# Kernel tuning notes

Measured on AMD Instinct MI355X. Metric: run time of the kernel, lower is better.

## Reference

```python
import jax, jax.numpy as jnp
import numpy as np

H = 1024
F = 4096  # base_ffn_dim = hidden * 4
WIDTHS = [256, 512]  # adapters; idx 2 -> width==hidden -> identity
EPS = 1e-5


def _xavier(key, fan_in, fan_out, gain):
    a = gain * np.sqrt(6.0 / (fan_in + fan_out))
    return jax.random.uniform(key, (fan_in, fan_out), jnp.float32, -a, a)


def _layernorm(x, g, b):
    mu = jnp.mean(x, axis=-1, keepdims=True)
    var = jnp.var(x, axis=-1, keepdims=True)
    return (x - mu) * jax.lax.rsqrt(var + EPS) * g + b


def setup_inputs() -> dict:
    key = jax.random.key(0)
    ks = jax.random.split(key, 12)
    g = 1.0 / np.sqrt(2.0)
    B, S = 4, 2048
    return {
        "x": jax.random.normal(ks[0], (B, S, H), jnp.float32),
        "width_multiplier": jax.random.uniform(ks[1], (B, S, 1), jnp.float32),
        "width_idx": jax.random.randint(ks[2], (B, S), 0, 3, jnp.int32),
        "ln_in_g": jnp.ones((H,), jnp.float32),
        "ln_in_b": jnp.zeros((H,), jnp.float32),
        "W1": _xavier(ks[3], H, F, g),
        "b1": jnp.zeros((F,), jnp.float32),
        "ln_h_g": jnp.ones((F,), jnp.float32),
        "ln_h_b": jnp.zeros((F,), jnp.float32),
        "W2": _xavier(ks[4], F, H, g),
        "b2": jnp.zeros((H,), jnp.float32),
        "a256_w1": _xavier(ks[5], H, 256, g),
        "a256_b1": jnp.zeros((256,), jnp.float32),
        "a256_w2": _xavier(ks[6], 256, H, g),
        "a256_b2": jnp.zeros((H,), jnp.float32),
        "a512_w1": _xavier(ks[7], H, 512, g),
        "a512_b1": jnp.zeros((512,), jnp.float32),
        "a512_w2": _xavier(ks[8], 512, H, g),
        "a512_b2": jnp.zeros((H,), jnp.float32),
    }


def reference(x, width_multiplier, width_idx,
              ln_in_g, ln_in_b, W1, b1, ln_h_g, ln_h_b, W2, b2,
              a256_w1, a256_b1, a256_w2, a256_b2,
              a512_w1, a512_b1, a512_w2, a512_b2):
    gelu = lambda t: jax.nn.gelu(t, approximate=False)  # torch nn.GELU exact
    x_norm = _layernorm(x, ln_in_g, ln_in_b)
    # base FFN path
    h = gelu(jnp.einsum("bsh,hf->bsf", x_norm, W1) + b1)
    h = _layernorm(h, ln_h_g, ln_h_b)
    base = jnp.einsum("bsf,fh->bsh", h, W2) + b2
    # width adapters (routed per token by width_idx)
    ad0 = jnp.einsum("bsw,wh->bsh", gelu(jnp.einsum("bsh,hw->bsw", x_norm, a256_w1) + a256_b1), a256_w2) + a256_b2
    ad1 = jnp.einsum("bsw,wh->bsh", gelu(jnp.einsum("bsh,hw->bsw", x_norm, a512_w1) + a512_b1), a512_w2) + a512_b2
    idx = width_idx[..., None]
    adaptive = jnp.where(idx == 0, ad0, jnp.where(idx == 1, ad1, x_norm))
    return base * width_multiplier + adaptive * (1.0 - width_multiplier)
```

## Files before the change

### kernel.cpp

```cpp
#include <hip/hip_runtime.h>
#include <cstdint>
#include <cstddef>

typedef unsigned short u16x8 __attribute__((ext_vector_type(8)));
typedef __bf16 bf16x8 __attribute__((ext_vector_type(8)));
typedef float f32x4 __attribute__((ext_vector_type(4)));

__device__ __forceinline__ float b2f(unsigned short u) {
    union { unsigned int i; float f; } v;
    v.i = ((unsigned int)u) << 16;
    return v.f;
}

__device__ __forceinline__ unsigned short f2b(float f) {
    union { float f; unsigned int i; } v;
    v.f = f;
    unsigned int x = v.i;
    unsigned int lsb = (x >> 16) & 1u;
    x += 0x7FFFu + lsb;
    return (unsigned short)(x >> 16);
}

__device__ __forceinline__ float gelu_exact(float x) {
    return 0.5f * x * (1.0f + erff(x * 0.70710678118654752f));
}

__global__ void transpose_f32_bf16(const float* __restrict__ in,
                                   unsigned short* __restrict__ out, int R, int C) {
    __shared__ float tile[32][33];
    int x = blockIdx.x * 32 + threadIdx.x;
    int y0 = blockIdx.y * 32;
    for (int k = 0; k < 32; k += 8)
        tile[threadIdx.y + k][threadIdx.x] = in[(size_t)(y0 + threadIdx.y + k) * C + x];
    __syncthreads();
    int ox = y0 + threadIdx.x;
    int oy = blockIdx.x * 32;
    for (int k = 0; k < 32; k += 8)
        out[(size_t)(oy + threadIdx.y + k) * R + ox] = f2b(tile[threadIdx.x][threadIdx.y + k]);
}

__device__ __forceinline__ float ldf(const float* p, int i) { return p[i]; }
__device__ __forceinline__ float ldf(const unsigned short* p, int i) { return b2f(p[i]); }

template <int NPT, typename TIN>
__global__ __launch_bounds__(256) void ln_rows(const TIN* __restrict__ in,
                                               unsigned short* __restrict__ out,
                                               const float* __restrict__ g,
                                               const float* __restrict__ b) {
    const int ncol = NPT * 256;
    const int row = blockIdx.x;
    const int t = threadIdx.x;
    const TIN* xr = in + (size_t)row * ncol;

    float v[NPT];
    float s = 0.f, s2 = 0.f;
#pragma unroll
    for (int i = 0; i < NPT; ++i) {
        float f = ldf(xr, t + (i << 8));
        v[i] = f;
        s += f;
        s2 += f * f;
    }
#pragma unroll
    for (int o = 32; o > 0; o >>= 1) {
        s  += __shfl_down(s, o, 64);
        s2 += __shfl_down(s2, o, 64);
    }
    __shared__ float red[8];
    int lane = t & 63, w = t >> 6;
    if (lane == 0) { red[w] = s; red[4 + w] = s2; }
    __syncthreads();
    if (t == 0) {
        red[0] = red[0] + red[1] + red[2] + red[3];
        red[4] = red[4] + red[5] + red[6] + red[7];
    }
    __syncthreads();
    float inv_n = 1.0f / (float)ncol;
    float mu = red[0] * inv_n;
    float var = red[4] * inv_n - mu * mu;
    float rs = rsqrtf(var + 1e-5f);

    unsigned short* orow = out + (size_t)row * ncol;
#pragma unroll
    for (int i = 0; i < NPT; ++i) {
        int c = t + (i << 8);
        orow[c] = f2b((v[i] - mu) * rs * g[c] + b[c]);
    }
}

#define LDSS 40

template <int EPI>
__global__ __launch_bounds__(256) void gemm_bt(
    const unsigned short* __restrict__ A, const unsigned short* __restrict__ BT,
    const float* __restrict__ bias, unsigned short* __restrict__ Cb,
    float* __restrict__ Cf, int M, int N, int K,
    const int* __restrict__ idx, int match,
    const float* __restrict__ wm,
    const unsigned short* __restrict__ adaptive,
    const unsigned short* __restrict__ xn) {
    __shared__ __align__(16) unsigned short As[128 * LDSS];
    __shared__ __align__(16) unsigned short Bs[128 * LDSS];

    const int t = threadIdx.x;
    const int m0 = blockIdx.y * 128;
    const int n0 = blockIdx.x * 128;

    const int r0 = t >> 2;
    const int kk = (t & 3) << 3;

    const int lane = t & 63;
    const int wid = t >> 6;
    const int wr = (wid >> 1) << 6;
    const int wc = (wid & 1) << 6;
    const int ml = lane & 15;
    const int q = lane >> 4;

    f32x4 acc[4][4];
#pragma unroll
    for (int i = 0; i < 4; ++i)
#pragma unroll
        for (int j = 0; j < 4; ++j)
#pragma unroll
            for (int r = 0; r < 4; ++r) acc[i][j][r] = 0.0f;

    for (int k0 = 0; k0 < K; k0 += 32) {
#pragma unroll
        for (int hh = 0; hh < 2; ++hh) {
            int row = r0 + (hh << 6);
            *(u16x8*)(&As[row * LDSS + kk]) =
                *(const u16x8*)(A + (size_t)(m0 + row) * K + k0 + kk);
            *(u16x8*)(&Bs[row * LDSS + kk]) =
                *(const u16x8*)(BT + (size_t)(n0 + row) * K + k0 + kk);
        }
        __syncthreads();

        bf16x8 af[4], bf[4];
#pragma unroll
        for (int i = 0; i < 4; ++i)
            af[i] = *(const bf16x8*)(&As[(wr + i * 16 + ml) * LDSS + (q << 3)]);
#pragma unroll
        for (int j = 0; j < 4; ++j)
            bf[j] = *(const bf16x8*)(&Bs[(wc + j * 16 + ml) * LDSS + (q << 3)]);
#pragma unroll
        for (int i = 0; i < 4; ++i)
#pragma unroll
            for (int j = 0; j < 4; ++j)
                acc[i][j] = __builtin_amdgcn_mfma_f32_16x16x32_bf16(af[i], bf[j], acc[i][j], 0, 0, 0);
        __syncthreads();
    }

#pragma unroll
    for (int i = 0; i < 4; ++i) {
#pragma unroll
        for (int j = 0; j < 4; ++j) {
            int col = n0 + wc + j * 16 + ml;
            float bv = bias[col];
#pragma unroll
            for (int r = 0; r < 4; ++r) {
                int row = m0 + wr + i * 16 + q * 4 + r;
                float val = acc[i][j][r] + bv;
                size_t off = (size_t)row * N + col;
                if (EPI == 0) {
                    Cb[off] = f2b(gelu_exact(val));
                } else if (EPI == 1) {
                    if (idx[row] == match) Cb[off] = f2b(val);
                } else {
                    float w = wm[row];
                    int id = idx[row];
                    float a = b2f((id <= 1) ? adaptive[off] : xn[off]);
                    Cf[off] = val * w + a * (1.0f - w);
                }
            }
        }
    }
}

extern "C" void kernel_launch(void* const* d_in, const int* in_sizes, int n_in,
                              void* d_out, int out_size, void* d_ws, size_t ws_size,
                              hipStream_t stream) {
    const float* x       = (const float*)d_in[0];
    const float* wm      = (const float*)d_in[1];
    const int*   widx    = (const int*)d_in[2];
    const float* ln_in_g = (const float*)d_in[3];
    const float* ln_in_b = (const float*)d_in[4];
    const float* W1      = (const float*)d_in[5];
    const float* b1      = (const float*)d_in[6];
    const float* ln_h_g  = (const float*)d_in[7];
    const float* ln_h_b  = (const float*)d_in[8];
    const float* W2      = (const float*)d_in[9];
    const float* b2      = (const float*)d_in[10];
    const float* a256_w1 = (const float*)d_in[11];
    const float* a256_b1 = (const float*)d_in[12];
    const float* a256_w2 = (const float*)d_in[13];
    const float* a256_b2 = (const float*)d_in[14];
    const float* a512_w1 = (const float*)d_in[15];
    const float* a512_b1 = (const float*)d_in[16];
    const float* a512_w2 = (const float*)d_in[17];
    const float* a512_b2 = (const float*)d_in[18];
    float* out = (float*)d_out;

    const int T = 8192, H = 1024, F = 4096;

    unsigned short* ws0   = (unsigned short*)d_ws;
    unsigned short* xn    = ws0;
    unsigned short* h     = xn    + (size_t)T * H;
    unsigned short* t0    = h     + (size_t)T * F;
    unsigned short* t1    = t0    + (size_t)T * 256;
    unsigned short* adp   = t1    + (size_t)T * 512;
    unsigned short* W1T   = adp   + (size_t)T * H;
    unsigned short* W2T   = W1T   + (size_t)H * F;
    unsigned short* aw1T0 = W2T   + (size_t)F * H;
    unsigned short* aw2T0 = aw1T0 + (size_t)256 * H;
    unsigned short* aw1T1 = aw2T0 + (size_t)H * 256;
    unsigned short* aw2T1 = aw1T1 + (size_t)512 * H;

    dim3 tb(32, 8);
    transpose_f32_bf16<<<dim3(F / 32,   H / 32), tb, 0, stream>>>(W1,      W1T,   H,   F);
    transpose_f32_bf16<<<dim3(H / 32,   F / 32), tb, 0, stream>>>(W2,      W2T,   F,   H);
    transpose_f32_bf16<<<dim3(256 / 32, H / 32), tb, 0, stream>>>(a256_w1, aw1T0, H,   256);
    transpose_f32_bf16<<<dim3(H / 32, 256 / 32), tb, 0, stream>>>(a256_w2, aw2T0, 256, H);
    transpose_f32_bf16<<<dim3(512 / 32, H / 32), tb, 0, stream>>>(a512_w1, aw1T1, H,   512);
    transpose_f32_bf16<<<dim3(H / 32, 512 / 32), tb, 0, stream>>>(a512_w2, aw2T1, 512, H);

    ln_rows<4, float><<<T, 256, 0, stream>>>(x, xn, ln_in_g, ln_in_b);

    gemm_bt<0><<<dim3(F / 128, T / 128), 256, 0, stream>>>(
        xn, W1T, b1, h, nullptr, T, F, H, nullptr, 0, nullptr, nullptr, nullptr);

    gemm_bt<0><<<dim3(256 / 128, T / 128), 256, 0, stream>>>(
        xn, aw1T0, a256_b1, t0, nullptr, T, 256, H, nullptr, 0, nullptr, nullptr, nullptr);
    gemm_bt<1><<<dim3(H / 128, T / 128), 256, 0, stream>>>(
        t0, aw2T0, a256_b2, adp, nullptr, T, H, 256, widx, 0, nullptr, nullptr, nullptr);

    gemm_bt<0><<<dim3(512 / 128, T / 128), 256, 0, stream>>>(
        xn, aw1T1, a512_b1, t1, nullptr, T, 512, H, nullptr, 0, nullptr, nullptr, nullptr);
    gemm_bt<1><<<dim3(H / 128, T / 128), 256, 0, stream>>>(
        t1, aw2T1, a512_b2, adp, nullptr, T, H, 512, widx, 1, nullptr, nullptr, nullptr);

    ln_rows<16, unsigned short><<<T, 256, 0, stream>>>(h, h, ln_h_g, ln_h_b);

    gemm_bt<2><<<dim3(H / 128, T / 128), 256, 0, stream>>>(
        h, W2T, b2, nullptr, out, T, H, F, widx, 0, wm, adp, xn);
}
```

Before: 507.3 us.

## Load GEMM tiles directly into LDS and fuse adapter up-projections

Global-to-shared tile loads in the GEMM now use the global_load_lds builtin, bypassing registers, and the padded LDS stride is replaced by an unpadded 32-element stride. Leading dimensions are passed as parameters so the two adapter up-projection GEMMs can be merged into a single N=768 GEMM, with the weights and biases concatenated. This aims to cut load instruction and register overhead and one kernel launch. The unpadded layout risks LDS bank conflicts on fragment reads.

```diff
diff --git a/kernel.cpp b/kernel.cpp
--- a/kernel.cpp
+++ b/kernel.cpp
@@ -23,6 +23,12 @@
 
 __device__ __forceinline__ float gelu_exact(float x) {
     return 0.5f * x * (1.0f + erff(x * 0.70710678118654752f));
+}
+
+__device__ __forceinline__ void ld_lds16(const unsigned short* g, unsigned short* l) {
+    __builtin_amdgcn_global_load_lds(
+        (const __attribute__((address_space(1))) void*)g,
+        (__attribute__((address_space(3))) void*)l, 16, 0, 0);
 }
 
 __global__ void transpose_f32_bf16(const float* __restrict__ in,
@@ -39,6 +45,13 @@
         out[(size_t)(oy + threadIdx.y + k) * R + ox] = f2b(tile[threadIdx.x][threadIdx.y + k]);
 }
 
+__global__ void concat_bias(const float* __restrict__ b0, const float* __restrict__ b1,
+                            float* __restrict__ out) {
+    int t = threadIdx.x + blockIdx.x * blockDim.x;
+    if (t < 256) out[t] = b0[t];
+    else if (t < 768) out[t] = b1[t - 256];
+}
+
 __device__ __forceinline__ float ldf(const float* p, int i) { return p[i]; }
 __device__ __forceinline__ float ldf(const unsigned short* p, int i) { return b2f(p[i]); }
 
@@ -88,29 +101,29 @@
     }
 }
 
-#define LDSS 40
-
 template <int EPI>
 __global__ __launch_bounds__(256) void gemm_bt(
-    const unsigned short* __restrict__ A, const unsigned short* __restrict__ BT,
+    const unsigned short* __restrict__ A, int lda,
+    const unsigned short* __restrict__ BT, int ldb,
     const float* __restrict__ bias, unsigned short* __restrict__ Cb,
     float* __restrict__ Cf, int M, int N, int K,
     const int* __restrict__ idx, int match,
     const float* __restrict__ wm,
     const unsigned short* __restrict__ adaptive,
     const unsigned short* __restrict__ xn) {
-    __shared__ __align__(16) unsigned short As[128 * LDSS];
-    __shared__ __align__(16) unsigned short Bs[128 * LDSS];
+    __shared__ __align__(16) unsigned short As[128 * 32];
+    __shared__ __align__(16) unsigned short Bs[128 * 32];
 
     const int t = threadIdx.x;
     const int m0 = blockIdx.y * 128;
     const int n0 = blockIdx.x * 128;
 
-    const int r0 = t >> 2;
-    const int kk = (t & 3) << 3;
-
     const int lane = t & 63;
     const int wid = t >> 6;
+
+    const int srow = lane >> 2;
+    const int scol = (lane & 3) << 3;
+
     const int wr = (wid >> 1) << 6;
     const int wc = (wid & 1) << 6;
     const int ml = lane & 15;
@@ -127,21 +140,20 @@
     for (int k0 = 0; k0 < K; k0 += 32) {
 #pragma unroll
         for (int hh = 0; hh < 2; ++hh) {
-            int row = r0 + (hh << 6);
-            *(u16x8*)(&As[row * LDSS + kk]) =
-                *(const u16x8*)(A + (size_t)(m0 + row) * K + k0 + kk);
-            *(u16x8*)(&Bs[row * LDSS + kk]) =
-                *(const u16x8*)(BT + (size_t)(n0 + row) * K + k0 + kk);
+            int rbase = wid * 32 + hh * 16;
+            int row = rbase + srow;
+            ld_lds16(A  + (size_t)(m0 + row) * lda + k0 + scol, &As[rbase * 32]);
+            ld_lds16(BT + (size_t)(n0 + row) * ldb + k0 + scol, &Bs[rbase * 32]);
         }
         __syncthreads();
 
         bf16x8 af[4], bf[4];
 #pragma unroll
         for (int i = 0; i < 4; ++i)
-            af[i] = *(const bf16x8*)(&As[(wr + i * 16 + ml) * LDSS + (q << 3)]);
+            af[i] = *(const bf16x8*)(&As[(wr + i * 16 + ml) * 32 + (q << 3)]);
 #pragma unroll
         for (int j = 0; j < 4; ++j)
-            bf[j] = *(const bf16x8*)(&Bs[(wc + j * 16 + ml) * LDSS + (q << 3)]);
+            bf[j] = *(const bf16x8*)(&Bs[(wc + j * 16 + ml) * 32 + (q << 3)]);
 #pragma unroll
         for (int i = 0; i < 4; ++i)
 #pragma unroll
@@ -205,41 +217,39 @@
     unsigned short* ws0   = (unsigned short*)d_ws;
     unsigned short* xn    = ws0;
     unsigned short* h     = xn    + (size_t)T * H;
-    unsigned short* t0    = h     + (size_t)T * F;
-    unsigned short* t1    = t0    + (size_t)T * 256;
-    unsigned short* adp   = t1    + (size_t)T * 512;
+    unsigned short* tt    = h     + (size_t)T * F;
+    unsigned short* adp   = tt    + (size_t)T * 768;
     unsigned short* W1T   = adp   + (size_t)T * H;
     unsigned short* W2T   = W1T   + (size_t)H * F;
-    unsigned short* aw1T0 = W2T   + (size_t)F * H;
-    unsigned short* aw2T0 = aw1T0 + (size_t)256 * H;
-    unsigned short* aw1T1 = aw2T0 + (size_t)H * 256;
-    unsigned short* aw2T1 = aw1T1 + (size_t)512 * H;
+    unsigned short* awup  = W2T   + (size_t)F * H;
+    unsigned short* aw2T0 = awup  + (size_t)768 * H;
+    unsigned short* aw2T1 = aw2T0 + (size_t)H * 256;
+    float*          ab1   = (float*)(aw2T1 + (size_t)H * 512);
 
     dim3 tb(32, 8);
-    transpose_f32_bf16<<<dim3(F / 32,   H / 32), tb, 0, stream>>>(W1,      W1T,   H,   F);
-    transpose_f32_bf16<<<dim3(H / 32,   F / 32), tb, 0, stream>>>(W2,      W2T,   F,   H);
-    transpose_f32_bf16<<<dim3(256 / 32, H / 32), tb, 0, stream>>>(a256_w1, aw1T0, H,   256);
+    transpose_f32_bf16<<<dim3(F / 32,   H / 32), tb, 0, stream>>>(W1, W1T, H, F);
+    transpose_f32_bf16<<<dim3(H / 32,   F / 32), tb, 0, stream>>>(W2, W2T, F, H);
+    transpose_f32_bf16<<<dim3(256 / 32, H / 32), tb, 0, stream>>>(a256_w1, awup, H, 256);
+    transpose_f32_bf16<<<dim3(512 / 32, H / 32), tb, 0, stream>>>(a512_w1, awup + (size_t)256 * H, H, 512);
     transpose_f32_bf16<<<dim3(H / 32, 256 / 32), tb, 0, stream>>>(a256_w2, aw2T0, 256, H);
-    transpose_f32_bf16<<<dim3(512 / 32, H / 32), tb, 0, stream>>>(a512_w1, aw1T1, H,   512);
     transpose_f32_bf16<<<dim3(H / 32, 512 / 32), tb, 0, stream>>>(a512_w2, aw2T1, 512, H);
+    concat_bias<<<3, 256, 0, stream>>>(a256_b1, a512_b1, ab1);
 
     ln_rows<4, float><<<T, 256, 0, stream>>>(x, xn, ln_in_g, ln_in_b);
 
     gemm_bt<0><<<dim3(F / 128, T / 128), 256, 0, stream>>>(
-        xn, W1T, b1, h, nullptr, T, F, H, nullptr, 0, nullptr, nullptr, nullptr);
-
-    gemm_bt<0><<<dim3(256 / 128, T / 128), 256, 0, stream>>>(
-        xn, aw1T0, a256_b1, t0, nullptr, T, 256, H, nullptr, 0, nullptr, nullptr, nullptr);
+        xn, H, W1T, H, b1, h, nullptr, T, F, H, nullptr, 0, nullptr, nullptr, nullptr);
+
+    gemm_bt<0><<<dim3(768 / 128, T / 128), 256, 0, stream>>>(
+        xn, H, awup, H, ab1, tt, nullptr, T, 768, H, nullptr, 0, nullptr, nullptr, nullptr);
+
     gemm_bt<1><<<dim3(H / 128, T / 128), 256, 0, stream>>>(
-        t0, aw2T0, a256_b2, adp, nullptr, T, H, 256, widx, 0, nullptr, nullptr, nullptr);
-
-    gemm_bt<0><<<dim3(512 / 128, T / 128), 256, 0, stream>>>(
-        xn, aw1T1, a512_b1, t1, nullptr, T, 512, H, nullptr, 0, nullptr, nullptr, nullptr);
+        tt, 768, aw2T0, 256, a256_b2, adp, nullptr, T, H, 256, widx, 0, nullptr, nullptr, nullptr);
     gemm_bt<1><<<dim3(H / 128, T / 128), 256, 0, stream>>>(
-        t1, aw2T1, a512_b2, adp, nullptr, T, H, 512, widx, 1, nullptr, nullptr, nullptr);
+        tt + 256, 768, aw2T1, 512, a512_b2, adp, nullptr, T, H, 512, widx, 1, nullptr, nullptr, nullptr);
 
     ln_rows<16, unsigned short><<<T, 256, 0, stream>>>(h, h, ln_h_g, ln_h_b);
 
     gemm_bt<2><<<dim3(H / 128, T / 128), 256, 0, stream>>>(
-        h, W2T, b2, nullptr, out, T, H, F, widx, 0, wm, adp, xn);
-}
+        h, F, W2T, F, b2, nullptr, out, T, H, F, widx, 0, wm, adp, xn);
+}
```

Result: faster. 474.3 us (-6.5%).
